# Optimization experiments

Hardware: AMD Instinct MI355X
Metric: run time of the kernel (lower is better)

The kernel has to match this reference:

```python
import jax, jax.numpy as jnp
import numpy as np
import math


def _favor(X, W, is_query):
    # X: [B,L,H,M], W: [M,M] (shared across batch, matching tf.repeat of a single QR matrix)
    M = X.shape[-1]
    dn = 1.0 / math.sqrt(math.sqrt(M))
    X = dn * X
    diag = (jnp.sum(X * X, axis=-1) * (0.5 * dn * dn))[..., None]  # [B,L,H,1]
    dot = jnp.einsum('dm,blhm->blhd', W, X)                         # [B,L,H,M]
    if is_query:
        mx = jnp.max(X, axis=-1, keepdims=True)
    else:
        mx = jnp.max(X, axis=(1, 3), keepdims=True)  # axes (-3,-1) = (L, M)
    return (1.0 / math.sqrt(M)) * jnp.exp(dot - diag - mx + 1e-8)


def _causal_attn(qs, ks, vs):
    # qs,ks: [B,L,H,M]; vs: [B,L,H,D]. Cumulative KV-state recurrence via lax.scan.
    B, L, H, M = ks.shape
    D = vs.shape[-1]

    def step(carry, x):
        sums, snorm = carry          # [B,H,M,D], [B,H,M]
        q, k, v = x                  # [B,H,M], [B,H,M], [B,H,D]
        snorm = snorm + k
        sums = sums + k[..., :, None] * v[..., None, :]
        num = jnp.einsum('bhmd,bhm->bhd', sums, q)
        den = jnp.sum(q * snorm, axis=-1, keepdims=True)
        return (sums, snorm), num / den

    init = (jnp.zeros((B, H, M, D), qs.dtype), jnp.zeros((B, H, M), qs.dtype))
    xs = (jnp.swapaxes(qs, 0, 1), jnp.swapaxes(ks, 0, 1), jnp.swapaxes(vs, 0, 1))
    _, out = jax.lax.scan(step, init, xs)   # out: [L,B,H,D]
    return jnp.swapaxes(out, 0, 1)          # [B,L,H,D]


def _make_favor_proj(rng, M):
    # Mirrors: W ~ N(0,1); Q,_ = qr(W); Q /= norm(Q, axis=-1) (TF broadcast divides columns); Q *= sqrt(M)
    W = rng.standard_normal((M, M)).astype(np.float32)
    Q, _ = np.linalg.qr(W)
    n = np.linalg.norm(Q, axis=1)          # row norms, shape (M,)
    Q = Q / n[None, :]                     # TF broadcasting quirk: divide column j by n[j]
    return jnp.asarray(Q * math.sqrt(M), dtype=jnp.float32)


def setup_inputs() -> dict:
    B, L, d_model, H = 2, 4096, 1024, 16
    M = d_model // H
    key = jax.random.key(0)
    k1, k2, k3 = jax.random.split(key, 3)
    rng = np.random.default_rng(0)

    def dense_w(dout):
        return jnp.asarray(rng.standard_normal((d_model, dout)).astype(np.float32) * 0.02)

    return {
        'queries': jax.random.normal(k1, (B, L, d_model), jnp.float32),
        'keys': jax.random.normal(k2, (B, L, d_model), jnp.float32),
        'values': jax.random.normal(k3, (B, L, d_model), jnp.float32),
        'Wq': dense_w(H * M), 'bq': jnp.zeros((H * M,), jnp.float32),
        'Wk': dense_w(H * M), 'bk': jnp.zeros((H * M,), jnp.float32),
        'Wv': dense_w(H * M), 'bv': jnp.zeros((H * M,), jnp.float32),
        'Wo': dense_w(d_model), 'bo': jnp.zeros((d_model,), jnp.float32),
        'Wfq': _make_favor_proj(rng, M),
        'Wfk': _make_favor_proj(rng, M),
        'H': H,
    }


def reference(queries, keys, values, Wq, bq, Wk, bk, Wv, bv, Wo, bo, Wfq, Wfk, H):
    N, L, _ = queries.shape
    S = keys.shape[1]
    q = (queries @ Wq + bq).reshape(N, L, H, -1)
    k = (keys @ Wk + bk).reshape(N, S, H, -1)
    v = (values @ Wv + bv).reshape(N, S, H, -1)
    Ql = _favor(q, Wfq, is_query=True)
    Kl = _favor(k, Wfk, is_query=False)
    V = _causal_attn(Ql, Kl, v)             # [N,L,H,D]
    return V.reshape(N, L, -1) @ Wo + bo    # [N,L,d_model]
```

## Files before the change

kernel.cpp:

```cpp
#include <hip/hip_runtime.h>
#include <math.h>

#define BATCH 2
#define SEQ   4096
#define DM    1024
#define NH    16
#define MD    64
#define NROW  (BATCH*SEQ)
#define RQ    (BATCH*SEQ*NH)
#define NCHUNK 64
#define CT     64
#define DN    0.35355339059327373f
#define INV_SQRT_M 0.125f
#define PITCH 72
#define STSZ  (65*64)
#define DIAG_SCALE (0.125f * 0.0625f)

typedef unsigned short ushort_t;
typedef short bf8_t __attribute__((ext_vector_type(8)));
typedef float f4_t  __attribute__((ext_vector_type(4)));
typedef ushort_t us8_t __attribute__((ext_vector_type(8)));

__device__ static inline ushort_t f2bf(float f) {
    union { float f; unsigned u; } v; v.f = f;
    unsigned r = v.u + 0x7FFFu + ((v.u >> 16) & 1u);
    return (ushort_t)(r >> 16);
}
__device__ static inline float bf2f(ushort_t u) {
    union { unsigned u; float f; } v; v.u = ((unsigned)u) << 16;
    return v.f;
}

__device__ static inline void async_ld16(const ushort_t* g, ushort_t* l) {
    __builtin_amdgcn_global_load_lds(
        (const __attribute__((address_space(1))) unsigned int*)g,
        (__attribute__((address_space(3))) unsigned int*)l,
        16, 0, 0);
}

__device__ static inline void sbar() {
    __builtin_amdgcn_sched_barrier(0);
    __builtin_amdgcn_s_barrier();
    __builtin_amdgcn_sched_barrier(0);
}
#define VMCNT(n) do { asm volatile("s_waitcnt vmcnt(" #n ")" ::: "memory"); \
                      __builtin_amdgcn_sched_barrier(0); } while (0)

__device__ static inline void gemm128_core(
    const ushort_t* __restrict__ A, const ushort_t* __restrict__ BT,
    ushort_t* As, ushort_t* Bs, int bm, int bn, int tid, f4_t acc[4][4])
{
    const int lane = tid & 63, w = tid >> 6;
    const int wr = w >> 2, wc = w & 3;
    const int quad = lane >> 4, l15 = lane & 15;
    const int lrow = lane >> 3;
    const int kcol = ((lane & 7) ^ lrow) * 8;

    auto stB = [&](int t, int s) {
        #pragma unroll
        for (int c = 0; c < 4; ++c) {
            const int r0 = c * 64 + w * 8;
            async_ld16(BT + (size_t)(bn + r0 + lrow) * DM + t * 64 + kcol,
                       &Bs[s * 16384 + r0 * 64]);
        }
    };
    auto stA1 = [&](int t, int s) {
        const int r0 = (w < 4) ? w * 8 : 32 + w * 8;
        async_ld16(A + (size_t)(bm + r0 + lrow) * DM + t * 64 + kcol,
                   &As[s * 8192 + r0 * 64]);
    };
    auto stA2 = [&](int t, int s) {
        const int r0 = (w < 4) ? 32 + w * 8 : 64 + w * 8;
        async_ld16(A + (size_t)(bm + r0 + lrow) * DM + t * 64 + kcol,
                   &As[s * 8192 + r0 * 64]);
    };

    auto loadB = [&](int s, bf8_t bf[2][4]) {
        #pragma unroll
        for (int ks = 0; ks < 2; ++ks) {
            const int slot8 = (((ks << 2) | quad) ^ (l15 & 7)) * 8;
            #pragma unroll
            for (int j = 0; j < 4; ++j) {
                const int row = wc * 64 + j * 16 + l15;
                bf[ks][j] = *(const bf8_t*)&Bs[s * 16384 + row * 64 + slot8];
            }
        }
    };
    auto loadA = [&](int s, int ih, bf8_t af[2][2]) {
        #pragma unroll
        for (int ks = 0; ks < 2; ++ks) {
            const int slot8 = (((ks << 2) | quad) ^ (l15 & 7)) * 8;
            #pragma unroll
            for (int i = 0; i < 2; ++i) {
                const int row = wr * 64 + (ih * 2 + i) * 16 + l15;
                af[ks][i] = *(const bf8_t*)&As[s * 8192 + row * 64 + slot8];
            }
        }
    };
    auto mfma16 = [&](int ih, bf8_t af[2][2], bf8_t bf[2][4]) {
        __builtin_amdgcn_s_setprio(1);
        #pragma unroll
        for (int ks = 0; ks < 2; ++ks)
            #pragma unroll
            for (int i = 0; i < 2; ++i)
                #pragma unroll
                for (int j = 0; j < 4; ++j)
                    acc[ih * 2 + i][j] = __builtin_amdgcn_mfma_f32_16x16x32_bf16(
                        af[ks][i], bf[ks][j], acc[ih * 2 + i][j], 0, 0, 0);
        __builtin_amdgcn_s_setprio(0);
    };

    stB(0, 0); stA1(0, 0);
    stA2(0, 0);
    stB(1, 1); stA1(1, 1);
    VMCNT(6);
    sbar();

    bf8_t bf[2][4], af[2][2];
    #pragma unroll 1
    for (int v = 0; v < 7; ++v) {
        const int u0 = 2 * v;
        loadB(0, bf); loadA(0, 0, af);
        stA2(u0 + 1, 1);
        VMCNT(6); sbar();
        mfma16(0, af, bf);
        sbar();
        loadA(0, 1, af);
        stB(u0 + 2, 0); stA1(u0 + 2, 0);
        VMCNT(6); sbar();
        mfma16(1, af, bf);
        sbar();
        loadB(1, bf); loadA(1, 0, af);
        stA2(u0 + 2, 0);
        VMCNT(6); sbar();
        mfma16(0, af, bf);
        sbar();
        loadA(1, 1, af);
        stB(u0 + 3, 1); stA1(u0 + 3, 1);
        VMCNT(6); sbar();
        mfma16(1, af, bf);
        sbar();
    }
    loadB(0, bf); loadA(0, 0, af);
    stA2(15, 1);
    VMCNT(6); sbar();
    mfma16(0, af, bf);
    sbar();
    loadA(0, 1, af);
    VMCNT(1); sbar();
    mfma16(1, af, bf);
    sbar();
    loadB(1, bf); loadA(1, 0, af);
    VMCNT(0); sbar();
    mfma16(0, af, bf);
    sbar();
    loadA(1, 1, af);
    mfma16(1, af, bf);
}

__device__ static inline void swz256(int bx, int* bm, int* bn) {
    const int xcd = bx & 7, s = bx >> 3;
    *bm = (xcd * 8 + (s >> 2)) << 7;
    *bn = (s & 3) << 8;
}

__global__ __launch_bounds__(256) void prep_weights(
    const float* __restrict__ W0, const float* __restrict__ W1,
    const float* __restrict__ W2, const float* __restrict__ W3,
    ushort_t* __restrict__ WT, unsigned* __restrict__ kmOrd)
{
    if (blockIdx.z == 0 && blockIdx.x == 0 && blockIdx.y == 0 && threadIdx.x < 32)
        kmOrd[threadIdx.x] = 0u;
    const float* W = blockIdx.z == 0 ? W0 : (blockIdx.z == 1 ? W1 : (blockIdx.z == 2 ? W2 : W3));
    ushort_t* dst = WT + (size_t)blockIdx.z * DM * DM;
    __shared__ float t[32][33];
    const int k0 = blockIdx.x * 32, n0 = blockIdx.y * 32;
    const int tx = threadIdx.x & 31, ty = threadIdx.x >> 5;
    #pragma unroll
    for (int r = 0; r < 32; r += 8)
        t[ty + r][tx] = W[(size_t)(k0 + ty + r) * 1024 + n0 + tx];
    __syncthreads();
    #pragma unroll
    for (int r = 0; r < 32; r += 8)
        dst[(size_t)(n0 + ty + r) * 1024 + k0 + tx] = f2bf(t[tx][ty + r]);
}

__global__ __launch_bounds__(256) void cvt_qkv(
    const float* __restrict__ Q, const float* __restrict__ K,
    const float* __restrict__ V, ushort_t* __restrict__ Y)
{
    const int y = blockIdx.y;
    const float* X = y == 0 ? Q : (y == 1 ? K : V);
    ushort_t* dst = Y + (size_t)y * NROW * DM;
    int i = blockIdx.x * 256 + threadIdx.x;
    const float4* X4 = (const float4*)X;
    float4 a = X4[i * 2], b = X4[i * 2 + 1];
    us8_t o;
    o[0]=f2bf(a.x); o[1]=f2bf(a.y); o[2]=f2bf(a.z); o[3]=f2bf(a.w);
    o[4]=f2bf(b.x); o[5]=f2bf(b.y); o[6]=f2bf(b.z); o[7]=f2bf(b.w);
    *(us8_t*)&dst[i * 8] = o;
}

__global__ __launch_bounds__(512, 2) void gemm_qkv(
    const ushort_t* __restrict__ Xc, const ushort_t* __restrict__ WT,
    const float* __restrict__ bq, const float* __restrict__ bk,
    const float* __restrict__ bv, ushort_t* __restrict__ Obase,
    unsigned* __restrict__ kmOrd)
{
    __shared__ ushort_t As[2 * 8192];
    __shared__ ushort_t Bs[2 * 16384];
    const int z = blockIdx.y;
    const ushort_t* A  = Xc + (size_t)z * NROW * DM;
    const ushort_t* BT = WT + (size_t)z * DM * DM;
    const float* bias = z == 0 ? bq : (z == 1 ? bk : bv);
    ushort_t* Cbf = Obase + (size_t)z * NROW * DM;

    const int tid = threadIdx.x;
    int bm, bn;
    swz256(blockIdx.x, &bm, &bn);
    const int lane = tid & 63, w = tid >> 6;
    const int wr = w >> 2, wc = w & 3;
    const int quad = lane >> 4, l15 = lane & 15;

    f4_t acc[4][4] = {};
    gemm128_core(A, BT, As, Bs, bm, bn, tid, acc);

    float mx = -3.4e38f;
    #pragma unroll
    for (int j = 0; j < 4; ++j) {
        const int col = bn + wc * 64 + j * 16 + l15;
        const float bb = bias[col];
        #pragma unroll
        for (int i = 0; i < 4; ++i) {
            const int row0 = bm + wr * 64 + i * 16 + quad * 4;
            #pragma unroll
            for (int r = 0; r < 4; ++r) {
                float v = acc[i][j][r] + bb;
                mx = fmaxf(mx, v);
                Cbf[(size_t)(row0 + r) * DM + col] = f2bf(v);
            }
        }
    }
    if (z == 1) {
        #pragma unroll
        for (int off = 32; off; off >>= 1) mx = fmaxf(mx, __shfl_xor(mx, off));
        if (lane == 0) {
            const int b = bm >> 12;
            const int h = (bn + wc * 64) >> 6;
            unsigned ub = __float_as_uint(mx);
            unsigned enc = (ub & 0x80000000u) ? ~ub : (ub | 0x80000000u);
            atomicMax(&kmOrd[b * NH + h], enc);
        }
    }
}

__global__ __launch_bounds__(512, 2) void gemm_out(
    const ushort_t* __restrict__ A, const ushort_t* __restrict__ BT,
    const float* __restrict__ bias, float* __restrict__ C)
{
    __shared__ ushort_t As[2 * 8192];
    __shared__ ushort_t Bs[2 * 16384];
    const int tid = threadIdx.x;
    int bm, bn;
    swz256(blockIdx.x, &bm, &bn);
    const int lane = tid & 63, w = tid >> 6;
    const int wr = w >> 2, wc = w & 3;
    const int quad = lane >> 4, l15 = lane & 15;

    f4_t acc[4][4] = {};
    gemm128_core(A, BT, As, Bs, bm, bn, tid, acc);

    #pragma unroll
    for (int j = 0; j < 4; ++j) {
        const int col = bn + wc * 64 + j * 16 + l15;
        const float bb = bias[col];
        #pragma unroll
        for (int i = 0; i < 4; ++i) {
            const int row0 = bm + wr * 64 + i * 16 + quad * 4;
            #pragma unroll
            for (int r = 0; r < 4; ++r)
                C[(size_t)(row0 + r) * DM + col] = acc[i][j][r] + bb;
        }
    }
}

__global__ __launch_bounds__(256) void favor_k_mfma(
    ushort_t* __restrict__ X, const float* __restrict__ Wf,
    const unsigned* __restrict__ kmOrd)
{
    __shared__ ushort_t Xs[64 * PITCH];
    __shared__ ushort_t Ws[64 * PITCH];
    __shared__ float ssp[64][4];
    __shared__ float diag[64], mxr[64];
    const int tid = threadIdx.x;
    const int lane = tid & 63, w = tid >> 6;
    const int quad = lane >> 4, l15 = lane & 15;
    const int rbase = blockIdx.x * 64;

    #pragma unroll
    for (int r = 0; r < 2; ++r) {
        int idx = tid + r * 256;
        int row = idx >> 3, ch = idx & 7;
        *(us8_t*)&Xs[row * PITCH + ch * 8] =
            *(const us8_t*)&X[(size_t)(rbase + row) * 64 + ch * 8];
    }
    const float4* Wf4 = (const float4*)Wf;
    #pragma unroll
    for (int i = 0; i < 4; ++i) {
        int f4i = tid + i * 256;
        int row = f4i >> 4, q4 = f4i & 15;
        float4 wv = Wf4[f4i];
        Ws[row * PITCH + q4 * 4 + 0] = f2bf(DN * wv.x);
        Ws[row * PITCH + q4 * 4 + 1] = f2bf(DN * wv.y);
        Ws[row * PITCH + q4 * 4 + 2] = f2bf(DN * wv.z);
        Ws[row * PITCH + q4 * 4 + 3] = f2bf(DN * wv.w);
    }
    __syncthreads();

    {
        const int row = tid >> 2, seg = tid & 3;
        const us8_t* xp = (const us8_t*)&Xs[row * PITCH + seg * 16];
        us8_t a = xp[0], b2 = xp[1];
        float ss = 0.f;
        #pragma unroll
        for (int j = 0; j < 8; ++j) {
            float x0 = bf2f(a[j]), x1 = bf2f(b2[j]);
            ss += x0 * x0 + x1 * x1;
        }
        ssp[row][seg] = ss;
    }
    __syncthreads();
    if (tid < 64) {
        diag[tid] = (ssp[tid][0] + ssp[tid][1] + ssp[tid][2] + ssp[tid][3]) * DIAG_SCALE;
        int rg = rbase + tid;
        int h = rg & (NH - 1);
        int b = rg >> 16;
        unsigned u = kmOrd[b * NH + h];
        unsigned bits = (u & 0x80000000u) ? (u & 0x7FFFFFFFu) : ~u;
        mxr[tid] = DN * __uint_as_float(bits);
    }
    __syncthreads();

    bf8_t xf[2];
    #pragma unroll
    for (int ks = 0; ks < 2; ++ks)
        xf[ks] = *(const bf8_t*)&Xs[(w * 16 + l15) * PITCH + ks * 32 + quad * 8];
    f4_t acc[4] = {};
    #pragma unroll
    for (int dt = 0; dt < 4; ++dt)
        #pragma unroll
        for (int ks = 0; ks < 2; ++ks) {
            bf8_t wfr = *(const bf8_t*)&Ws[(dt * 16 + l15) * PITCH + ks * 32 + quad * 8];
            acc[dt] = __builtin_amdgcn_mfma_f32_16x16x32_bf16(xf[ks], wfr, acc[dt], 0, 0, 0);
        }
    __syncthreads();

    #pragma unroll
    for (int r = 0; r < 4; ++r) {
        int row = w * 16 + quad * 4 + r;
        float d_ = diag[row], m_ = mxr[row];
        #pragma unroll
        for (int dt = 0; dt < 4; ++dt) {
            float e = acc[dt][r] - d_ - m_ + 1e-8f;
            X[(size_t)(rbase + row) * 64 + dt * 16 + l15] = f2bf(INV_SQRT_M * expf(e));
        }
    }
}

__global__ __launch_bounds__(256) void chunk_sums_mfma(
    const ushort_t* __restrict__ Kbf, const ushort_t* __restrict__ Vbf,
    ushort_t* __restrict__ ST)
{
    const int bx = blockIdx.x;
    const int c = bx & 63, h = (bx >> 6) & 15, b = bx >> 10;
    __shared__ ushort_t Kt[64 * PITCH];
    __shared__ ushort_t Vt[80 * PITCH];
    const int tid = threadIdx.x;
    const int lane = tid & 63, w = tid >> 6;
    const int quad = lane >> 4, l15 = lane & 15;

    const size_t gbase = ((size_t)(b * SEQ + c * CT)) * DM + h * MD;
    #pragma unroll
    for (int r = 0; r < 2; ++r) {
        int ch = w + r * 4;
        int t = lane;
        us8_t kv = *(const us8_t*)&Kbf[gbase + (size_t)t * DM + ch * 8];
        us8_t vv = *(const us8_t*)&Vbf[gbase + (size_t)t * DM + ch * 8];
        #pragma unroll
        for (int j = 0; j < 8; ++j) {
            Kt[(ch * 8 + j) * PITCH + t] = kv[j];
            Vt[(ch * 8 + j) * PITCH + t] = vv[j];
        }
    }
    if (tid < 64) Vt[64 * PITCH + tid] = (ushort_t)0x3F80;
    __syncthreads();

    ushort_t* Sg = ST + (size_t)((b * NH + h) * NCHUNK + c) * STSZ;

    bf8_t vf[2];
    #pragma unroll
    for (int ks = 0; ks < 2; ++ks)
        vf[ks] = *(const bf8_t*)&Vt[(w * 16 + l15) * PITCH + ks * 32 + quad * 8];
    f4_t acc[4] = {};
    #pragma unroll
    for (int mt = 0; mt < 4; ++mt)
        #pragma unroll
        for (int ks = 0; ks < 2; ++ks) {
            bf8_t kf = *(const bf8_t*)&Kt[(mt * 16 + l15) * PITCH + ks * 32 + quad * 8];
            acc[mt] = __builtin_amdgcn_mfma_f32_16x16x32_bf16(vf[ks], kf, acc[mt], 0, 0, 0);
        }
    #pragma unroll
    for (int mt = 0; mt < 4; ++mt)
        #pragma unroll
        for (int r = 0; r < 4; ++r)
            Sg[(w * 16 + quad * 4 + r) * 64 + mt * 16 + l15] = f2bf(acc[mt][r]);

    if (w == 0) {
        bf8_t vf4[2];
        #pragma unroll
        for (int ks = 0; ks < 2; ++ks)
            vf4[ks] = *(const bf8_t*)&Vt[(64 + l15) * PITCH + ks * 32 + quad * 8];
        f4_t accz[4] = {};
        #pragma unroll
        for (int mt = 0; mt < 4; ++mt)
            #pragma unroll
            for (int ks = 0; ks < 2; ++ks) {
                bf8_t kf = *(const bf8_t*)&Kt[(mt * 16 + l15) * PITCH + ks * 32 + quad * 8];
                accz[mt] = __builtin_amdgcn_mfma_f32_16x16x32_bf16(vf4[ks], kf, accz[mt], 0, 0, 0);
            }
        if (quad == 0) {
            #pragma unroll
            for (int mt = 0; mt < 4; ++mt)
                Sg[64 * 64 + mt * 16 + l15] = f2bf(accz[mt][0]);
        }
    }
}

__global__ __launch_bounds__(256) void prefix_scan_st(ushort_t* __restrict__ ST)
{
    const int sb = blockIdx.x / 17;
    const int e = (blockIdx.x % 17) * 256 + threadIdx.x;
    if (e >= STSZ) return;
    ushort_t* p = ST + (size_t)sb * NCHUNK * STSZ + e;
    ushort_t v[NCHUNK];
    #pragma unroll
    for (int c = 0; c < NCHUNK; ++c) v[c] = p[(size_t)c * STSZ];
    float run = 0.f;
    #pragma unroll
    for (int c = 0; c < NCHUNK; ++c) {
        float cur = bf2f(v[c]);
        p[(size_t)c * STSZ] = f2bf(run);
        run += cur;
    }
}

__global__ __launch_bounds__(256) void intra_attn_mfma(
    const ushort_t* __restrict__ Qraw, const ushort_t* __restrict__ Kbf,
    const ushort_t* __restrict__ Vbf, const ushort_t* __restrict__ ST,
    const float* __restrict__ Wfq, ushort_t* __restrict__ Obf)
{
    const int bx = blockIdx.x;
    const int c = bx & 63, h = (bx >> 6) & 15, b = bx >> 10;
    __shared__ ushort_t Qs[64 * PITCH];
    __shared__ ushort_t Ks[64 * PITCH];
    __shared__ ushort_t Vt[80 * PITCH];
    __shared__ ushort_t St[80 * PITCH];
    __shared__ ushort_t Ws[64 * PITCH];
    __shared__ float ssp[64][4];
    __shared__ float mxp[64][4];
    __shared__ float diag[64], mxr[64], dens[64];
    const int tid = threadIdx.x;
    const int lane = tid & 63, w = tid >> 6;
    const int quad = lane >> 4, l15 = lane & 15;

    const size_t gbase = ((size_t)(b * SEQ + c * CT)) * DM + h * MD;

    #pragma unroll
    for (int r = 0; r < 2; ++r) {
        int idx = tid + r * 256;
        int row = idx >> 3, ch = idx & 7;
        us8_t qv = *(const us8_t*)&Qraw[gbase + (size_t)row * DM + ch * 8];
        us8_t kv = *(const us8_t*)&Kbf[gbase + (size_t)row * DM + ch * 8];
        *(us8_t*)&Qs[row * PITCH + ch * 8] = qv;
        *(us8_t*)&Ks[row * PITCH + ch * 8] = kv;
    }
    #pragma unroll
    for (int r = 0; r < 2; ++r) {
        int ch = w + r * 4;
        int t = lane;
        us8_t vv = *(const us8_t*)&Vbf[gbase + (size_t)t * DM + ch * 8];
        #pragma unroll
        for (int j = 0; j < 8; ++j) Vt[(ch * 8 + j) * PITCH + t] = vv[j];
    }
    #pragma unroll
    for (int r = 0; r < 4; ++r) {
        int idx = tid + r * 256;
        int row = 64 + (idx >> 6), t = idx & 63;
        Vt[row * PITCH + t] = (row == 64) ? (ushort_t)0x3F80 : (ushort_t)0;
    }
    const us8_t* Sg8 = (const us8_t*)(ST + (size_t)((b * NH + h) * NCHUNK + c) * STSZ);
    #pragma unroll
    for (int r = 0; r < 3; ++r) {
        int idx = tid + r * 256;
        if (idx < 520) {
            int d = idx >> 3, mo = (idx & 7) * 8;
            *(us8_t*)&St[d * PITCH + mo] = Sg8[idx];
        }
        int idx2 = idx - 520;
        if (idx2 >= 0 && idx2 < 120) {
            int row = 65 + (idx2 >> 3), mo = (idx2 & 7) * 8;
            us8_t z = {};
            *(us8_t*)&St[row * PITCH + mo] = z;
        }
    }
    const float4* Wf4 = (const float4*)Wfq;
    #pragma unroll
    for (int i = 0; i < 4; ++i) {
        int f4i = tid + i * 256;
        int row = f4i >> 4, q4 = f4i & 15;
        float4 wv = Wf4[f4i];
        Ws[row * PITCH + q4 * 4 + 0] = f2bf(DN * wv.x);
        Ws[row * PITCH + q4 * 4 + 1] = f2bf(DN * wv.y);
        Ws[row * PITCH + q4 * 4 + 2] = f2bf(DN * wv.z);
        Ws[row * PITCH + q4 * 4 + 3] = f2bf(DN * wv.w);
    }
    __syncthreads();

    {
        const int row = tid >> 2, seg = tid & 3;
        const us8_t* xp = (const us8_t*)&Qs[row * PITCH + seg * 16];
        us8_t a = xp[0], b2 = xp[1];
        float ss = 0.f, mx = -3.4e38f;
        #pragma unroll
        for (int j = 0; j < 8; ++j) {
            float x0 = bf2f(a[j]), x1 = bf2f(b2[j]);
            ss += x0 * x0 + x1 * x1;
            mx = fmaxf(mx, fmaxf(x0, x1));
        }
        ssp[row][seg] = ss;
        mxp[row][seg] = mx;
    }
    __syncthreads();
    if (tid < 64) {
        diag[tid] = (ssp[tid][0] + ssp[tid][1] + ssp[tid][2] + ssp[tid][3]) * DIAG_SCALE;
        mxr[tid] = DN * fmaxf(fmaxf(mxp[tid][0], mxp[tid][1]),
                              fmaxf(mxp[tid][2], mxp[tid][3]));
    }
    __syncthreads();

    {
        bf8_t xf[2];
        #pragma unroll
        for (int ks = 0; ks < 2; ++ks)
            xf[ks] = *(const bf8_t*)&Qs[(w * 16 + l15) * PITCH + ks * 32 + quad * 8];
        f4_t facc[4] = {};
        #pragma unroll
        for (int dt = 0; dt < 4; ++dt)
            #pragma unroll
            for (int ks = 0; ks < 2; ++ks) {
                bf8_t wfr = *(const bf8_t*)&Ws[(dt * 16 + l15) * PITCH + ks * 32 + quad * 8];
                facc[dt] = __builtin_amdgcn_mfma_f32_16x16x32_bf16(xf[ks], wfr, facc[dt], 0, 0, 0);
            }
        __syncthreads();
        #pragma unroll
        for (int r = 0; r < 4; ++r) {
            int row = w * 16 + quad * 4 + r;
            float d_ = diag[row], m_ = mxr[row];
            #pragma unroll
            for (int dt = 0; dt < 4; ++dt) {
                float e = facc[dt][r] - d_ - m_ + 1e-8f;
                Qs[row * PITCH + dt * 16 + l15] = f2bf(INV_SQRT_M * expf(e));
            }
        }
    }
    __syncthreads();

    bf8_t qf[2];
    #pragma unroll
    for (int ks = 0; ks < 2; ++ks)
        qf[ks] = *(const bf8_t*)&Qs[(w * 16 + l15) * PITCH + ks * 32 + quad * 8];
    f4_t accA[4] = {};
    #pragma unroll
    for (int jt = 0; jt < 4; ++jt)
        #pragma unroll
        for (int ks = 0; ks < 2; ++ks) {
            bf8_t kf = *(const bf8_t*)&Ks[(jt * 16 + l15) * PITCH + ks * 32 + quad * 8];
            accA[jt] = __builtin_amdgcn_mfma_f32_16x16x32_bf16(qf[ks], kf, accA[jt], 0, 0, 0);
        }
    __syncthreads();
    #pragma unroll
    for (int jt = 0; jt < 4; ++jt) {
        int j = jt * 16 + l15;
        #pragma unroll
        for (int r = 0; r < 4; ++r) {
            int i = w * 16 + quad * 4 + r;
            float a = (j <= i) ? accA[jt][r] : 0.f;
            Ks[i * PITCH + j] = f2bf(a);
        }
    }
    __syncthreads();

    bf8_t af[2];
    #pragma unroll
    for (int ks = 0; ks < 2; ++ks)
        af[ks] = *(const bf8_t*)&Ks[(w * 16 + l15) * PITCH + ks * 32 + quad * 8];
    f4_t acc[5] = {};
    #pragma unroll
    for (int dt = 0; dt < 5; ++dt)
        #pragma unroll
        for (int ks = 0; ks < 2; ++ks) {
            bf8_t sf = *(const bf8_t*)&St[(dt * 16 + l15) * PITCH + ks * 32 + quad * 8];
            acc[dt] = __builtin_amdgcn_mfma_f32_16x16x32_bf16(qf[ks], sf, acc[dt], 0, 0, 0);
            bf8_t vf = *(const bf8_t*)&Vt[(dt * 16 + l15) * PITCH + ks * 32 + quad * 8];
            acc[dt] = __builtin_amdgcn_mfma_f32_16x16x32_bf16(af[ks], vf, acc[dt], 0, 0, 0);
        }
    if (l15 == 0) {
        #pragma unroll
        for (int r = 0; r < 4; ++r) dens[w * 16 + quad * 4 + r] = acc[4][r];
    }
    __syncthreads();

    #pragma unroll
    for (int r = 0; r < 4; ++r) {
        int i = w * 16 + quad * 4 + r;
        float inv = 1.0f / dens[i];
        #pragma unroll
        for (int dt = 0; dt < 4; ++dt)
            Obf[gbase + (size_t)i * DM + dt * 16 + l15] = f2bf(acc[dt][r] * inv);
    }
}

extern "C" void kernel_launch(void* const* d_in, const int* in_sizes, int n_in,
                              void* d_out, int out_size, void* d_ws, size_t ws_size,
                              hipStream_t stream)
{
    const float* queries = (const float*)d_in[0];
    const float* keys    = (const float*)d_in[1];
    const float* values  = (const float*)d_in[2];
    const float* Wq = (const float*)d_in[3];  const float* bq = (const float*)d_in[4];
    const float* Wk = (const float*)d_in[5];  const float* bk = (const float*)d_in[6];
    const float* Wv = (const float*)d_in[7];  const float* bv = (const float*)d_in[8];
    const float* Wo = (const float*)d_in[9];  const float* bo = (const float*)d_in[10];
    const float* Wfq = (const float*)d_in[11];
    const float* Wfk = (const float*)d_in[12];

    char* ws = (char*)d_ws;
    unsigned* kmOrd = (unsigned*)ws;
    ushort_t* STb = (ushort_t*)(ws + 256);
    ushort_t* qbf = STb + (size_t)32 * NCHUNK * STSZ;
    ushort_t* kbf = qbf + (size_t)NROW * DM;
    ushort_t* vbf = kbf + (size_t)NROW * DM;
    ushort_t* obf = vbf + (size_t)NROW * DM;
    ushort_t* xcvt = obf + (size_t)NROW * DM;
    ushort_t* wT  = xcvt + (size_t)3 * NROW * DM;
    ushort_t* WoT = wT + (size_t)3 * DM * DM;

    prep_weights<<<dim3(32, 32, 4), 256, 0, stream>>>(Wq, Wk, Wv, Wo, wT, kmOrd);

    const int n8 = NROW * DM / 8;
    cvt_qkv<<<dim3(n8 / 256, 3), 256, 0, stream>>>(queries, keys, values, xcvt);

    gemm_qkv<<<dim3(256, 3), 512, 0, stream>>>(xcvt, wT, bq, bk, bv, qbf, kmOrd);

    favor_k_mfma<<<RQ / 64, 256, 0, stream>>>(kbf, Wfk, kmOrd);

    chunk_sums_mfma<<<BATCH * NH * NCHUNK, 256, 0, stream>>>(kbf, vbf, STb);
    prefix_scan_st<<<32 * 17, 256, 0, stream>>>(STb);
    intra_attn_mfma<<<BATCH * NH * NCHUNK, 256, 0, stream>>>(qbf, kbf, vbf, STb, Wfq, obf);

    gemm_out<<<256, 512, 0, stream>>>(obf, WoT, bo, (float*)d_out);
}
```

Before: 319.3 us.

## Fuse fp32-to-bf16 input conversion into the QKV GEMM A-tile loads

```diff
diff --git a/kernel.cpp b/kernel.cpp
--- a/kernel.cpp
+++ b/kernel.cpp
@@ -45,6 +45,17 @@
 }
 #define VMCNT(n) do { asm volatile("s_waitcnt vmcnt(" #n ")" ::: "memory"); \
                       __builtin_amdgcn_sched_barrier(0); } while (0)
+#define LGKM0() do { asm volatile("s_waitcnt lgkmcnt(0)" ::: "memory"); \
+                     __builtin_amdgcn_sched_barrier(0); } while (0)
+
+__device__ static inline void swz256(int bx, int* bm, int* bn) {
+    const int xcd = bx & 7, s = bx >> 3;
+    *bm = (xcd * 8 + (s >> 2)) << 7;
+    *bn = (s & 3) << 8;
+}
+
+#define ABUF (128*64)
+#define BBUF (256*64)
 
 __device__ static inline void gemm128_core(
     const ushort_t* __restrict__ A, const ushort_t* __restrict__ BT,
@@ -61,18 +72,18 @@
         for (int c = 0; c < 4; ++c) {
             const int r0 = c * 64 + w * 8;
             async_ld16(BT + (size_t)(bn + r0 + lrow) * DM + t * 64 + kcol,
-                       &Bs[s * 16384 + r0 * 64]);
+                       &Bs[s * BBUF + r0 * 64]);
         }
     };
     auto stA1 = [&](int t, int s) {
         const int r0 = (w < 4) ? w * 8 : 32 + w * 8;
         async_ld16(A + (size_t)(bm + r0 + lrow) * DM + t * 64 + kcol,
-                   &As[s * 8192 + r0 * 64]);
+                   &As[s * ABUF + r0 * 64]);
     };
     auto stA2 = [&](int t, int s) {
         const int r0 = (w < 4) ? 32 + w * 8 : 64 + w * 8;
         async_ld16(A + (size_t)(bm + r0 + lrow) * DM + t * 64 + kcol,
-                   &As[s * 8192 + r0 * 64]);
+                   &As[s * ABUF + r0 * 64]);
     };
 
     auto loadB = [&](int s, bf8_t bf[2][4]) {
@@ -82,7 +93,7 @@
             #pragma unroll
             for (int j = 0; j < 4; ++j) {
                 const int row = wc * 64 + j * 16 + l15;
-                bf[ks][j] = *(const bf8_t*)&Bs[s * 16384 + row * 64 + slot8];
+                bf[ks][j] = *(const bf8_t*)&Bs[s * BBUF + row * 64 + slot8];
             }
         }
     };
@@ -93,7 +104,7 @@
             #pragma unroll
             for (int i = 0; i < 2; ++i) {
                 const int row = wr * 64 + (ih * 2 + i) * 16 + l15;
-                af[ks][i] = *(const bf8_t*)&As[s * 8192 + row * 64 + slot8];
+                af[ks][i] = *(const bf8_t*)&As[s * ABUF + row * 64 + slot8];
             }
         }
     };
@@ -158,12 +169,6 @@
     mfma16(1, af, bf);
 }
 
-__device__ static inline void swz256(int bx, int* bm, int* bn) {
-    const int xcd = bx & 7, s = bx >> 3;
-    *bm = (xcd * 8 + (s >> 2)) << 7;
-    *bn = (s & 3) << 8;
-}
-
 __global__ __launch_bounds__(256) void prep_weights(
     const float* __restrict__ W0, const float* __restrict__ W1,
     const float* __restrict__ W2, const float* __restrict__ W3,
@@ -185,32 +190,17 @@
         dst[(size_t)(n0 + ty + r) * 1024 + k0 + tx] = f2bf(t[tx][ty + r]);
 }
 
-__global__ __launch_bounds__(256) void cvt_qkv(
-    const float* __restrict__ Q, const float* __restrict__ K,
-    const float* __restrict__ V, ushort_t* __restrict__ Y)
-{
-    const int y = blockIdx.y;
-    const float* X = y == 0 ? Q : (y == 1 ? K : V);
-    ushort_t* dst = Y + (size_t)y * NROW * DM;
-    int i = blockIdx.x * 256 + threadIdx.x;
-    const float4* X4 = (const float4*)X;
-    float4 a = X4[i * 2], b = X4[i * 2 + 1];
-    us8_t o;
-    o[0]=f2bf(a.x); o[1]=f2bf(a.y); o[2]=f2bf(a.z); o[3]=f2bf(a.w);
-    o[4]=f2bf(b.x); o[5]=f2bf(b.y); o[6]=f2bf(b.z); o[7]=f2bf(b.w);
-    *(us8_t*)&dst[i * 8] = o;
-}
-
 __global__ __launch_bounds__(512, 2) void gemm_qkv(
-    const ushort_t* __restrict__ Xc, const ushort_t* __restrict__ WT,
+    const float* __restrict__ Qf, const float* __restrict__ Kf,
+    const float* __restrict__ Vf, const ushort_t* __restrict__ WT,
     const float* __restrict__ bq, const float* __restrict__ bk,
     const float* __restrict__ bv, ushort_t* __restrict__ Obase,
     unsigned* __restrict__ kmOrd)
 {
-    __shared__ ushort_t As[2 * 8192];
-    __shared__ ushort_t Bs[2 * 16384];
+    __shared__ ushort_t As[2 * ABUF];
+    __shared__ ushort_t Bs[2 * BBUF];
     const int z = blockIdx.y;
-    const ushort_t* A  = Xc + (size_t)z * NROW * DM;
+    const float* A32 = z == 0 ? Qf : (z == 1 ? Kf : Vf);
     const ushort_t* BT = WT + (size_t)z * DM * DM;
     const float* bias = z == 0 ? bq : (z == 1 ? bk : bv);
     ushort_t* Cbf = Obase + (size_t)z * NROW * DM;
@@ -221,9 +211,87 @@
     const int lane = tid & 63, w = tid >> 6;
     const int wr = w >> 2, wc = w & 3;
     const int quad = lane >> 4, l15 = lane & 15;
-
+    const int lrow = lane >> 3;
+    const int kcol = ((lane & 7) ^ lrow) * 8;
+
+    const int arow = tid >> 2, aseg = tid & 3;
+    const float* gA = A32 + (size_t)(bm + arow) * DM + aseg * 16;
+    const int ws0 = ((aseg * 2) ^ (arow & 7)) * 8;
+    const int ws1 = ((aseg * 2 + 1) ^ (arow & 7)) * 8;
+
+    f4_t a0, a1, a2, a3;
+    auto issueA = [&](int t) {
+        const f4_t* p = (const f4_t*)(gA + t * 64);
+        a0 = p[0]; a1 = p[1]; a2 = p[2]; a3 = p[3];
+    };
+    auto cvtWriteA = [&](int sel) {
+        us8_t o0, o1;
+        o0[0]=f2bf(a0[0]); o0[1]=f2bf(a0[1]); o0[2]=f2bf(a0[2]); o0[3]=f2bf(a0[3]);
+        o0[4]=f2bf(a1[0]); o0[5]=f2bf(a1[1]); o0[6]=f2bf(a1[2]); o0[7]=f2bf(a1[3]);
+        o1[0]=f2bf(a2[0]); o1[1]=f2bf(a2[1]); o1[2]=f2bf(a2[2]); o1[3]=f2bf(a2[3]);
+        o1[4]=f2bf(a3[0]); o1[5]=f2bf(a3[1]); o1[6]=f2bf(a3[2]); o1[7]=f2bf(a3[3]);
+        *(us8_t*)&As[sel * ABUF + arow * 64 + ws0] = o0;
+        *(us8_t*)&As[sel * ABUF + arow * 64 + ws1] = o1;
+    };
+    auto stB = [&](int t, int s) {
+        #pragma unroll
+        for (int c = 0; c < 4; ++c) {
+            const int r0 = c * 64 + w * 8;
+            async_ld16(BT + (size_t)(bn + r0 + lrow) * DM + t * 64 + kcol,
+                       &Bs[s * BBUF + r0 * 64]);
+        }
+    };
+
+    bf8_t af[4], bf[4];
+    auto rdFrags = [&](int s, int ks) {
+        const int slot8 = (((ks << 2) | quad) ^ (l15 & 7)) * 8;
+        #pragma unroll
+        for (int i = 0; i < 4; ++i)
+            af[i] = *(const bf8_t*)&As[s * ABUF + (wr * 64 + i * 16 + l15) * 64 + slot8];
+        #pragma unroll
+        for (int j = 0; j < 4; ++j)
+            bf[j] = *(const bf8_t*)&Bs[s * BBUF + (wc * 64 + j * 16 + l15) * 64 + slot8];
+    };
     f4_t acc[4][4] = {};
-    gemm128_core(A, BT, As, Bs, bm, bn, tid, acc);
+    auto mm = [&]() {
+        __builtin_amdgcn_s_setprio(1);
+        #pragma unroll
+        for (int i = 0; i < 4; ++i)
+            #pragma unroll
+            for (int j = 0; j < 4; ++j)
+                acc[i][j] = __builtin_amdgcn_mfma_f32_16x16x32_bf16(
+                    af[i], bf[j], acc[i][j], 0, 0, 0);
+        __builtin_amdgcn_s_setprio(0);
+    };
+
+    issueA(0);
+    VMCNT(0);
+    cvtWriteA(0);
+    stB(0, 0);
+    LGKM0();
+
+    #pragma unroll 1
+    for (int t = 0; t < 15; ++t) {
+        const int s = t & 1;
+        issueA(t + 1);
+        VMCNT(4);
+        sbar();
+        rdFrags(s, 0);
+        stB(t + 1, s ^ 1);
+        mm();
+        VMCNT(4);
+        cvtWriteA(s ^ 1);
+        rdFrags(s, 1);
+        mm();
+        LGKM0();
+        sbar();
+    }
+    VMCNT(0);
+    sbar();
+    rdFrags(1, 0);
+    mm();
+    rdFrags(1, 1);
+    mm();
 
     float mx = -3.4e38f;
     #pragma unroll
@@ -258,8 +326,8 @@
     const ushort_t* __restrict__ A, const ushort_t* __restrict__ BT,
     const float* __restrict__ bias, float* __restrict__ C)
 {
-    __shared__ ushort_t As[2 * 8192];
-    __shared__ ushort_t Bs[2 * 16384];
+    __shared__ ushort_t As[2 * ABUF];
+    __shared__ ushort_t Bs[2 * BBUF];
     const int tid = threadIdx.x;
     int bm, bn;
     swz256(blockIdx.x, &bm, &bn);
@@ -651,16 +719,13 @@
     ushort_t* kbf = qbf + (size_t)NROW * DM;
     ushort_t* vbf = kbf + (size_t)NROW * DM;
     ushort_t* obf = vbf + (size_t)NROW * DM;
-    ushort_t* xcvt = obf + (size_t)NROW * DM;
-    ushort_t* wT  = xcvt + (size_t)3 * NROW * DM;
+    ushort_t* wT  = obf + (size_t)NROW * DM;
     ushort_t* WoT = wT + (size_t)3 * DM * DM;
 
     prep_weights<<<dim3(32, 32, 4), 256, 0, stream>>>(Wq, Wk, Wv, Wo, wT, kmOrd);
 
-    const int n8 = NROW * DM / 8;
-    cvt_qkv<<<dim3(n8 / 256, 3), 256, 0, stream>>>(queries, keys, values, xcvt);
-
-    gemm_qkv<<<dim3(256, 3), 512, 0, stream>>>(xcvt, wT, bq, bk, bv, qbf, kmOrd);
+    gemm_qkv<<<dim3(256, 3), 512, 0, stream>>>(queries, keys, values, wT,
+                                               bq, bk, bv, qbf, kmOrd);
 
     favor_k_mfma<<<RQ / 64, 256, 0, stream>>>(kbf, Wfk, kmOrd);
 
```

New measurement: 328.2 us. 1.03x slower.

## Fuse key FAVOR feature map into chunk-sum and intra-attention kernels

Applied to the files above, without the earlier changes.

```diff
diff --git a/kernel.cpp b/kernel.cpp
--- a/kernel.cpp
+++ b/kernel.cpp
@@ -46,6 +46,15 @@
 #define VMCNT(n) do { asm volatile("s_waitcnt vmcnt(" #n ")" ::: "memory"); \
                       __builtin_amdgcn_sched_barrier(0); } while (0)
 
+__device__ static inline void swz256(int bx, int* bm, int* bn) {
+    const int xcd = bx & 7, s = bx >> 3;
+    *bm = (xcd * 8 + (s >> 2)) << 7;
+    *bn = (s & 3) << 8;
+}
+
+#define ABUF (128*64)
+#define BBUF (256*64)
+
 __device__ static inline void gemm128_core(
     const ushort_t* __restrict__ A, const ushort_t* __restrict__ BT,
     ushort_t* As, ushort_t* Bs, int bm, int bn, int tid, f4_t acc[4][4])
@@ -61,18 +70,18 @@
         for (int c = 0; c < 4; ++c) {
             const int r0 = c * 64 + w * 8;
             async_ld16(BT + (size_t)(bn + r0 + lrow) * DM + t * 64 + kcol,
-                       &Bs[s * 16384 + r0 * 64]);
+                       &Bs[s * BBUF + r0 * 64]);
         }
     };
     auto stA1 = [&](int t, int s) {
         const int r0 = (w < 4) ? w * 8 : 32 + w * 8;
         async_ld16(A + (size_t)(bm + r0 + lrow) * DM + t * 64 + kcol,
-                   &As[s * 8192 + r0 * 64]);
+                   &As[s * ABUF + r0 * 64]);
     };
     auto stA2 = [&](int t, int s) {
         const int r0 = (w < 4) ? 32 + w * 8 : 64 + w * 8;
         async_ld16(A + (size_t)(bm + r0 + lrow) * DM + t * 64 + kcol,
-                   &As[s * 8192 + r0 * 64]);
+                   &As[s * ABUF + r0 * 64]);
     };
 
     auto loadB = [&](int s, bf8_t bf[2][4]) {
@@ -82,7 +91,7 @@
             #pragma unroll
             for (int j = 0; j < 4; ++j) {
                 const int row = wc * 64 + j * 16 + l15;
-                bf[ks][j] = *(const bf8_t*)&Bs[s * 16384 + row * 64 + slot8];
+                bf[ks][j] = *(const bf8_t*)&Bs[s * BBUF + row * 64 + slot8];
             }
         }
     };
@@ -93,7 +102,7 @@
             #pragma unroll
             for (int i = 0; i < 2; ++i) {
                 const int row = wr * 64 + (ih * 2 + i) * 16 + l15;
-                af[ks][i] = *(const bf8_t*)&As[s * 8192 + row * 64 + slot8];
+                af[ks][i] = *(const bf8_t*)&As[s * ABUF + row * 64 + slot8];
             }
         }
     };
@@ -158,12 +167,6 @@
     mfma16(1, af, bf);
 }
 
-__device__ static inline void swz256(int bx, int* bm, int* bn) {
-    const int xcd = bx & 7, s = bx >> 3;
-    *bm = (xcd * 8 + (s >> 2)) << 7;
-    *bn = (s & 3) << 8;
-}
-
 __global__ __launch_bounds__(256) void prep_weights(
     const float* __restrict__ W0, const float* __restrict__ W1,
     const float* __restrict__ W2, const float* __restrict__ W3,
@@ -207,8 +210,8 @@
     const float* __restrict__ bv, ushort_t* __restrict__ Obase,
     unsigned* __restrict__ kmOrd)
 {
-    __shared__ ushort_t As[2 * 8192];
-    __shared__ ushort_t Bs[2 * 16384];
+    __shared__ ushort_t As[2 * ABUF];
+    __shared__ ushort_t Bs[2 * BBUF];
     const int z = blockIdx.y;
     const ushort_t* A  = Xc + (size_t)z * NROW * DM;
     const ushort_t* BT = WT + (size_t)z * DM * DM;
@@ -258,8 +261,8 @@
     const ushort_t* __restrict__ A, const ushort_t* __restrict__ BT,
     const float* __restrict__ bias, float* __restrict__ C)
 {
-    __shared__ ushort_t As[2 * 8192];
-    __shared__ ushort_t Bs[2 * 16384];
+    __shared__ ushort_t As[2 * ABUF];
+    __shared__ ushort_t Bs[2 * BBUF];
     const int tid = threadIdx.x;
     int bm, bn;
     swz256(blockIdx.x, &bm, &bn);
@@ -284,27 +287,42 @@
     }
 }
 
-__global__ __launch_bounds__(256) void favor_k_mfma(
-    ushort_t* __restrict__ X, const float* __restrict__ Wf,
-    const unsigned* __restrict__ kmOrd)
-{
-    __shared__ ushort_t Xs[64 * PITCH];
+__global__ __launch_bounds__(256) void chunk_sums_mfma(
+    const ushort_t* __restrict__ Kbf, const ushort_t* __restrict__ Vbf,
+    const float* __restrict__ Wfk, const unsigned* __restrict__ kmOrd,
+    ushort_t* __restrict__ ST)
+{
+    const int bx = blockIdx.x;
+    const int c = bx & 63, h = (bx >> 6) & 15, b = bx >> 10;
+    __shared__ ushort_t Ks[64 * PITCH];
+    __shared__ ushort_t Kt[64 * PITCH];
+    __shared__ ushort_t Vt[80 * PITCH];
     __shared__ ushort_t Ws[64 * PITCH];
     __shared__ float ssp[64][4];
-    __shared__ float diag[64], mxr[64];
+    __shared__ float diag[64];
     const int tid = threadIdx.x;
     const int lane = tid & 63, w = tid >> 6;
     const int quad = lane >> 4, l15 = lane & 15;
-    const int rbase = blockIdx.x * 64;
+
+    const size_t gbase = ((size_t)(b * SEQ + c * CT)) * DM + h * MD;
 
     #pragma unroll
     for (int r = 0; r < 2; ++r) {
         int idx = tid + r * 256;
         int row = idx >> 3, ch = idx & 7;
-        *(us8_t*)&Xs[row * PITCH + ch * 8] =
-            *(const us8_t*)&X[(size_t)(rbase + row) * 64 + ch * 8];
-    }
-    const float4* Wf4 = (const float4*)Wf;
+        *(us8_t*)&Ks[row * PITCH + ch * 8] =
+            *(const us8_t*)&Kbf[gbase + (size_t)row * DM + ch * 8];
+    }
+    #pragma unroll
+    for (int r = 0; r < 2; ++r) {
+        int ch = w + r * 4;
+        int t = lane;
+        us8_t vv = *(const us8_t*)&Vbf[gbase + (size_t)t * DM + ch * 8];
+        #pragma unroll
+        for (int j = 0; j < 8; ++j) Vt[(ch * 8 + j) * PITCH + t] = vv[j];
+    }
+    if (tid < 64) Vt[64 * PITCH + tid] = (ushort_t)0x3F80;
+    const float4* Wf4 = (const float4*)Wfk;
     #pragma unroll
     for (int i = 0; i < 4; ++i) {
         int f4i = tid + i * 256;
@@ -319,7 +337,7 @@
 
     {
         const int row = tid >> 2, seg = tid & 3;
-        const us8_t* xp = (const us8_t*)&Xs[row * PITCH + seg * 16];
+        const us8_t* xp = (const us8_t*)&Ks[row * PITCH + seg * 16];
         us8_t a = xp[0], b2 = xp[1];
         float ss = 0.f;
         #pragma unroll
@@ -330,69 +348,37 @@
         ssp[row][seg] = ss;
     }
     __syncthreads();
-    if (tid < 64) {
+    if (tid < 64)
         diag[tid] = (ssp[tid][0] + ssp[tid][1] + ssp[tid][2] + ssp[tid][3]) * DIAG_SCALE;
-        int rg = rbase + tid;
-        int h = rg & (NH - 1);
-        int b = rg >> 16;
-        unsigned u = kmOrd[b * NH + h];
-        unsigned bits = (u & 0x80000000u) ? (u & 0x7FFFFFFFu) : ~u;
-        mxr[tid] = DN * __uint_as_float(bits);
-    }
-    __syncthreads();
-
-    bf8_t xf[2];
-    #pragma unroll
-    for (int ks = 0; ks < 2; ++ks)
-        xf[ks] = *(const bf8_t*)&Xs[(w * 16 + l15) * PITCH + ks * 32 + quad * 8];
-    f4_t acc[4] = {};
-    #pragma unroll
-    for (int dt = 0; dt < 4; ++dt)
-        #pragma unroll
-        for (int ks = 0; ks < 2; ++ks) {
-            bf8_t wfr = *(const bf8_t*)&Ws[(dt * 16 + l15) * PITCH + ks * 32 + quad * 8];
-            acc[dt] = __builtin_amdgcn_mfma_f32_16x16x32_bf16(xf[ks], wfr, acc[dt], 0, 0, 0);
-        }
-    __syncthreads();
-
-    #pragma unroll
-    for (int r = 0; r < 4; ++r) {
-        int row = w * 16 + quad * 4 + r;
-        float d_ = diag[row], m_ = mxr[row];
-        #pragma unroll
-        for (int dt = 0; dt < 4; ++dt) {
-            float e = acc[dt][r] - d_ - m_ + 1e-8f;
-            X[(size_t)(rbase + row) * 64 + dt * 16 + l15] = f2bf(INV_SQRT_M * expf(e));
-        }
-    }
-}
-
-__global__ __launch_bounds__(256) void chunk_sums_mfma(
-    const ushort_t* __restrict__ Kbf, const ushort_t* __restrict__ Vbf,
-    ushort_t* __restrict__ ST)
-{
-    const int bx = blockIdx.x;
-    const int c = bx & 63, h = (bx >> 6) & 15, b = bx >> 10;
-    __shared__ ushort_t Kt[64 * PITCH];
-    __shared__ ushort_t Vt[80 * PITCH];
-    const int tid = threadIdx.x;
-    const int lane = tid & 63, w = tid >> 6;
-    const int quad = lane >> 4, l15 = lane & 15;
-
-    const size_t gbase = ((size_t)(b * SEQ + c * CT)) * DM + h * MD;
-    #pragma unroll
-    for (int r = 0; r < 2; ++r) {
-        int ch = w + r * 4;
-        int t = lane;
-        us8_t kv = *(const us8_t*)&Kbf[gbase + (size_t)t * DM + ch * 8];
-        us8_t vv = *(const us8_t*)&Vbf[gbase + (size_t)t * DM + ch * 8];
-        #pragma unroll
-        for (int j = 0; j < 8; ++j) {
-            Kt[(ch * 8 + j) * PITCH + t] = kv[j];
-            Vt[(ch * 8 + j) * PITCH + t] = vv[j];
-        }
-    }
-    if (tid < 64) Vt[64 * PITCH + tid] = (ushort_t)0x3F80;
+    unsigned u = kmOrd[b * NH + h];
+    unsigned bits = (u & 0x80000000u) ? (u & 0x7FFFFFFFu) : ~u;
+    const float mxs = DN * __uint_as_float(bits);
+    __syncthreads();
+
+    {
+        bf8_t xf[2];
+        #pragma unroll
+        for (int ks = 0; ks < 2; ++ks)
+            xf[ks] = *(const bf8_t*)&Ks[(w * 16 + l15) * PITCH + ks * 32 + quad * 8];
+        f4_t facc[4] = {};
+        #pragma unroll
+        for (int dt = 0; dt < 4; ++dt)
+            #pragma unroll
+            for (int ks = 0; ks < 2; ++ks) {
+                bf8_t wfr = *(const bf8_t*)&Ws[(dt * 16 + l15) * PITCH + ks * 32 + quad * 8];
+                facc[dt] = __builtin_amdgcn_mfma_f32_16x16x32_bf16(xf[ks], wfr, facc[dt], 0, 0, 0);
+            }
+        #pragma unroll
+        for (int r = 0; r < 4; ++r) {
+            int t = w * 16 + quad * 4 + r;
+            float d_ = diag[t];
+            #pragma unroll
+            for (int dt = 0; dt < 4; ++dt) {
+                float e = facc[dt][r] - d_ - mxs + 1e-8f;
+                Kt[(dt * 16 + l15) * PITCH + t] = f2bf(INV_SQRT_M * expf(e));
+            }
+        }
+    }
     __syncthreads();
 
     ushort_t* Sg = ST + (size_t)((b * NH + h) * NCHUNK + c) * STSZ;
@@ -457,7 +443,8 @@
 __global__ __launch_bounds__(256) void intra_attn_mfma(
     const ushort_t* __restrict__ Qraw, const ushort_t* __restrict__ Kbf,
     const ushort_t* __restrict__ Vbf, const ushort_t* __restrict__ ST,
-    const float* __restrict__ Wfq, ushort_t* __restrict__ Obf)
+    const float* __restrict__ Wfq, const float* __restrict__ Wfk,
+    const unsigned* __restrict__ kmOrd, ushort_t* __restrict__ Obf)
 {
     const int bx = blockIdx.x;
     const int c = bx & 63, h = (bx >> 6) & 15, b = bx >> 10;
@@ -513,12 +500,12 @@
             *(us8_t*)&St[row * PITCH + mo] = z;
         }
     }
-    const float4* Wf4 = (const float4*)Wfq;
+    const float4* Wq4 = (const float4*)Wfq;
     #pragma unroll
     for (int i = 0; i < 4; ++i) {
         int f4i = tid + i * 256;
         int row = f4i >> 4, q4 = f4i & 15;
-        float4 wv = Wf4[f4i];
+        float4 wv = Wq4[f4i];
         Ws[row * PITCH + q4 * 4 + 0] = f2bf(DN * wv.x);
         Ws[row * PITCH + q4 * 4 + 1] = f2bf(DN * wv.y);
         Ws[row * PITCH + q4 * 4 + 2] = f2bf(DN * wv.z);
@@ -570,6 +557,64 @@
             for (int dt = 0; dt < 4; ++dt) {
                 float e = facc[dt][r] - d_ - m_ + 1e-8f;
                 Qs[row * PITCH + dt * 16 + l15] = f2bf(INV_SQRT_M * expf(e));
+            }
+        }
+    }
+    __syncthreads();
+
+    const float4* Wk4 = (const float4*)Wfk;
+    #pragma unroll
+    for (int i = 0; i < 4; ++i) {
+        int f4i = tid + i * 256;
+        int row = f4i >> 4, q4 = f4i & 15;
+        float4 wv = Wk4[f4i];
+        Ws[row * PITCH + q4 * 4 + 0] = f2bf(DN * wv.x);
+        Ws[row * PITCH + q4 * 4 + 1] = f2bf(DN * wv.y);
+        Ws[row * PITCH + q4 * 4 + 2] = f2bf(DN * wv.z);
+        Ws[row * PITCH + q4 * 4 + 3] = f2bf(DN * wv.w);
+    }
+    {
+        const int row = tid >> 2, seg = tid & 3;
+        const us8_t* xp = (const us8_t*)&Ks[row * PITCH + seg * 16];
+        us8_t a = xp[0], b2 = xp[1];
+        float ss = 0.f;
+        #pragma unroll
+        for (int j = 0; j < 8; ++j) {
+            float x0 = bf2f(a[j]), x1 = bf2f(b2[j]);
+            ss += x0 * x0 + x1 * x1;
+        }
+        ssp[row][seg] = ss;
+    }
+    __syncthreads();
+    if (tid < 64)
+        diag[tid] = (ssp[tid][0] + ssp[tid][1] + ssp[tid][2] + ssp[tid][3]) * DIAG_SCALE;
+    unsigned ku = kmOrd[b * NH + h];
+    unsigned kbits = (ku & 0x80000000u) ? (ku & 0x7FFFFFFFu) : ~ku;
+    const float mxs = DN * __uint_as_float(kbits);
+    __syncthreads();
+
+    {
+        bf8_t xf[2];
+        #pragma unroll
+        for (int ks = 0; ks < 2; ++ks)
+            xf[ks] = *(const bf8_t*)&Ks[(w * 16 + l15) * PITCH + ks * 32 + quad * 8];
+        f4_t facc[4] = {};
+        #pragma unroll
+        for (int dt = 0; dt < 4; ++dt)
+            #pragma unroll
+            for (int ks = 0; ks < 2; ++ks) {
+                bf8_t wfr = *(const bf8_t*)&Ws[(dt * 16 + l15) * PITCH + ks * 32 + quad * 8];
+                facc[dt] = __builtin_amdgcn_mfma_f32_16x16x32_bf16(xf[ks], wfr, facc[dt], 0, 0, 0);
+            }
+        __syncthreads();
+        #pragma unroll
+        for (int r = 0; r < 4; ++r) {
+            int row = w * 16 + quad * 4 + r;
+            float d_ = diag[row];
+            #pragma unroll
+            for (int dt = 0; dt < 4; ++dt) {
+                float e = facc[dt][r] - d_ - mxs + 1e-8f;
+                Ks[row * PITCH + dt * 16 + l15] = f2bf(INV_SQRT_M * expf(e));
             }
         }
     }
@@ -662,11 +707,10 @@
 
     gemm_qkv<<<dim3(256, 3), 512, 0, stream>>>(xcvt, wT, bq, bk, bv, qbf, kmOrd);
 
-    favor_k_mfma<<<RQ / 64, 256, 0, stream>>>(kbf, Wfk, kmOrd);
-
-    chunk_sums_mfma<<<BATCH * NH * NCHUNK, 256, 0, stream>>>(kbf, vbf, STb);
+    chunk_sums_mfma<<<BATCH * NH * NCHUNK, 256, 0, stream>>>(kbf, vbf, Wfk, kmOrd, STb);
     prefix_scan_st<<<32 * 17, 256, 0, stream>>>(STb);
-    intra_attn_mfma<<<BATCH * NH * NCHUNK, 256, 0, stream>>>(qbf, kbf, vbf, STb, Wfq, obf);
+    intra_attn_mfma<<<BATCH * NH * NCHUNK, 256, 0, stream>>>(qbf, kbf, vbf, STb,
+                                                             Wfq, Wfk, kmOrd, obf);
 
     gemm_out<<<256, 512, 0, stream>>>(obf, WoT, bo, (float*)d_out);
 }
```

New measurement: 313.3 us. About the same (-1.9%).
